# Kernel optimization log

Measured on AMD Instinct MI355X. Metric: run time of the kernel, lower is better.

The kernel has to match this reference:

```python
import jax, jax.numpy as jnp
import numpy as np

B, N, K = 4, 1024, 512
HEADS, DH = 8, 64
HID = 2048
KAPPA = 1.0      # kappa_beta
ALPHA = 1e-3     # ffn_alpha (prior weight)
LAM = 1.0        # ffn_lambda_belief
NITER = 2        # ffn_n_iterations
EPS = 1e-8


def _ln(x, g, b):
    m = jnp.mean(x, axis=-1, keepdims=True)
    v = jnp.var(x, axis=-1, keepdims=True)
    return (x - m) * jax.lax.rsqrt(v + 1e-5) * g + b


def _transport(x, phi, G):
    # truncated exp(phi . G) applied to x without materializing (B,N,K,K)
    def Ax(y):
        return jnp.einsum('bng,gkl,bnl->bnk', phi, G, y)
    a1 = Ax(x)
    return x + a1 + 0.5 * Ax(a1)


def setup_inputs() -> dict:
    key = jax.random.key(0)
    ks = jax.random.split(key, 16)
    mu_q = jax.random.normal(ks[0], (B, N, K), dtype=jnp.float32)
    sigma_q = jax.random.uniform(ks[1], (B, N, K), minval=0.5, maxval=1.5, dtype=jnp.float32)
    phi = 0.1 * jax.random.normal(ks[2], (B, N, 3), dtype=jnp.float32)
    A = jax.random.normal(ks[3], (3, K, K), dtype=jnp.float32)
    generators = 0.05 * (A - jnp.transpose(A, (0, 2, 1)))  # antisymmetric Lie generators
    mask = jnp.broadcast_to(jnp.tril(jnp.ones((N, N), dtype=bool)), (B, N, N))  # causal
    mu_prior = jax.random.normal(ks[4], (B, N, K), dtype=jnp.float32)
    s = 0.02
    Wq = s * jax.random.normal(ks[5], (K, K), dtype=jnp.float32)
    Wk = s * jax.random.normal(ks[6], (K, K), dtype=jnp.float32)
    Wv = s * jax.random.normal(ks[7], (K, K), dtype=jnp.float32)
    Wo = s * jax.random.normal(ks[8], (K, K), dtype=jnp.float32)
    g1 = jnp.ones((K,), jnp.float32); be1 = jnp.zeros((K,), jnp.float32)
    g2 = jnp.ones((K,), jnp.float32); be2 = jnp.zeros((K,), jnp.float32)
    W1 = s * jax.random.normal(ks[9], (K, HID), dtype=jnp.float32)
    bh1 = jnp.zeros((HID,), jnp.float32)
    W2 = s * jax.random.normal(ks[10], (HID, K), dtype=jnp.float32)
    bh2 = jnp.zeros((K,), jnp.float32)
    lr = jnp.array(0.1, jnp.float32)  # learnable VFE step size
    return {'mu_q': mu_q, 'sigma_q': sigma_q, 'phi': phi, 'generators': generators,
            'mask': mask, 'mu_prior': mu_prior, 'Wq': Wq, 'Wk': Wk, 'Wv': Wv, 'Wo': Wo,
            'g1': g1, 'be1': be1, 'g2': g2, 'be2': be2,
            'W1': W1, 'bh1': bh1, 'W2': W2, 'bh2': bh2, 'lr': lr}


def reference(mu_q, sigma_q, phi, generators, mask, mu_prior,
              Wq, Wk, Wv, Wo, g1, be1, g2, be2, W1, bh1, W2, bh2, lr):
    # ---- attention sublayer ----
    mu_n = _ln(mu_q, g1, be1)
    mu_g = _transport(mu_n, phi, generators)  # transport to common frame

    def heads(x):  # (B,N,K) -> (B,H,N,Dh)
        return x.reshape(B, N, HEADS, DH).transpose(0, 2, 1, 3)

    q = heads(mu_g @ Wq)
    k = heads(mu_g @ Wk)
    v = heads(mu_g @ Wv)
    # diagonal covariance propagated through linear maps: var_out = sigma @ W^2
    sq = heads(sigma_q @ (Wq * Wq)) + EPS
    sk = heads(sigma_q @ (Wk * Wk)) + EPS

    inv = 1.0 / sq
    # KL(N(k_j,sk_j) || N(q_i,sq_i)) for diagonal Gaussians, decomposed into matmuls
    tr = jnp.einsum('bhid,bhjd->bhij', inv, sk)
    quad = (jnp.sum(q * q * inv, axis=-1)[..., None]
            - 2.0 * jnp.einsum('bhid,bhjd->bhij', q * inv, k)
            + jnp.einsum('bhid,bhjd->bhij', inv, k * k))
    logdet = (jnp.sum(jnp.log(sq), axis=-1)[..., None]
              - jnp.sum(jnp.log(sk), axis=-1)[:, :, None, :])
    kl = 0.5 * (tr + quad - DH + logdet)  # (B,H,N,N)

    scores = jnp.where(mask[:, None, :, :], -kl / KAPPA, -1e9)
    beta = jax.nn.softmax(scores, axis=-1)

    out = jnp.einsum('bhij,bhjd->bhid', beta, v)
    out = out.transpose(0, 2, 1, 3).reshape(B, N, K)
    mu_attn = _transport(out @ Wo, -phi, generators)  # back-transport to local frames
    mu_res = mu_q + mu_attn  # residual (dropout is identity in eval)

    # ---- VFE_dynamic FFN sublayer ----
    mu_n2 = _ln(mu_res, g2, be2)
    beta_m = jnp.mean(beta, axis=1)  # (B,N,N) attention-belief coupling
    h = mu_n2
    for _ in range(NITER):
        drive = jax.nn.gelu(h @ W1 + bh1) @ W2 + bh2
        grad = ALPHA * (h - mu_prior) + LAM * (h - jnp.einsum('bij,bjk->bik', beta_m, h))
        h = h + lr * (drive - grad)
    mu_out = mu_res + (h - mu_n2)

    return (mu_out, sigma_q, phi)
```

## Files before the change

### kernel.cpp

```cpp
#include <hip/hip_runtime.h>
#include <math.h>

#define BB 4
#define NN 1024
#define KK 512
#define HH 8
#define DHh 64
#define HIDd 2048
#define BN (BB*NN)

typedef unsigned short u16;
typedef __attribute__((ext_vector_type(8))) short bf16x8;
typedef __attribute__((ext_vector_type(4))) float f32x4;

__device__ __forceinline__ float gelu_tanh(float x){
    float x3 = x*x*x;
    float t = tanhf(0.7978845608028654f*(x + 0.044715f*x3));
    return 0.5f*x*(1.0f+t);
}
__device__ __forceinline__ u16 f2bf(float x){
    unsigned int u = __float_as_uint(x);
    unsigned int r = (u + 0x7fffu + ((u>>16)&1u)) >> 16;
    return (u16)r;
}
__device__ __forceinline__ float bf2f(u16 b){
    return __uint_as_float(((unsigned int)b)<<16);
}
__device__ __forceinline__ void gload16(const void* g, void* l){
    __builtin_amdgcn_global_load_lds((__attribute__((address_space(1))) void*)g,
                                     (__attribute__((address_space(3))) void*)l, 16, 0, 0);
}
__device__ __forceinline__ void wsplit(u16* hi, u16* lo, size_t o, float v){
    u16 h = f2bf(v);
    hi[o] = h;
    if (lo) lo[o] = f2bf(v - bf2f(h));
}

__global__ __launch_bounds__(256) void split_t_k(
    const float* __restrict__ src, u16* __restrict__ hi, u16* __restrict__ lo,
    int Kc, int Nc, long sS, long sD, int square)
{
    __shared__ float t[32][33];
    const int n0 = blockIdx.x*32, k0 = blockIdx.y*32, bz = blockIdx.z;
    const float* S = src + (long)bz*sS;
    const int tx = threadIdx.x & 31, ty = threadIdx.x >> 5;
    for (int r = ty; r < 32; r += 8){
        float v = S[(long)(k0+r)*Nc + n0+tx];
        if (square) v *= v;
        t[r][tx] = v;
    }
    __syncthreads();
    for (int r = ty; r < 32; r += 8){
        float v = t[tx][r];
        long o = (long)bz*sD + (long)(n0+r)*Kc + k0 + tx;
        wsplit(hi, lo, o, v);
    }
}

__global__ __launch_bounds__(256) void wmega_k(
    const float* __restrict__ Wq, const float* __restrict__ Wk,
    const float* __restrict__ Wv, const float* __restrict__ Wo,
    const float* __restrict__ W1, const float* __restrict__ W2,
    const float* __restrict__ gen,
    u16* __restrict__ WQKVh, u16* __restrict__ WQKVl, u16* __restrict__ WoTh,
    u16* __restrict__ WSQKh, u16* __restrict__ WSQKl,
    u16* __restrict__ W1Th, u16* __restrict__ W2Th, u16* __restrict__ GFh)
{
    const int z = blockIdx.z;
    const int tid = threadIdx.x;
    if (z == 8){
        if (blockIdx.x >= 48) return;
        const int c0 = blockIdx.x*32, k0 = blockIdx.y*32;
        const int tx = tid&31, ty = tid>>5;
        const int g = c0/KK, l0 = c0%KK;
        for (int r=ty; r<32; r+=8)
            GFh[(size_t)(k0+r)*(3*KK) + c0+tx] =
                f2bf(gen[(size_t)g*KK*KK + (size_t)(k0+r)*KK + l0+tx]);
        return;
    }
    __shared__ float t[32][33];
    const float* src; u16* hi; u16* lo=0; int sq=0;
    int n0, k0, Kc, Nc;
    const size_t KK2 = (size_t)KK*KK;
    if (z < 6){
        if (blockIdx.x >= 16) return;
        n0 = blockIdx.x*32; k0 = blockIdx.y*32; Kc=KK; Nc=KK;
        if      (z==0){ src=Wq; hi=WQKVh;       lo=WQKVl; }
        else if (z==1){ src=Wk; hi=WQKVh+KK2;   lo=WQKVl+KK2; }
        else if (z==2){ src=Wv; hi=WQKVh+2*KK2; lo=WQKVl+2*KK2; }
        else if (z==3){ src=Wo; hi=WoTh; }
        else if (z==4){ src=Wq; hi=WSQKh;       lo=WSQKl; sq=1; }
        else          { src=Wk; hi=WSQKh+KK2;   lo=WSQKl+KK2; sq=1; }
    } else if (z == 6){
        src=W1; hi=W1Th; Kc=KK; Nc=HIDd;
        n0 = blockIdx.x*32; k0 = blockIdx.y*32;
    } else {
        src=W2; hi=W2Th; Kc=HIDd; Nc=KK;
        n0 = blockIdx.y*32; k0 = blockIdx.x*32;
    }
    const int tx=tid&31, ty=tid>>5;
    for (int r=ty;r<32;r+=8){
        float v = src[(long)(k0+r)*Nc + n0+tx];
        if (sq) v*=v;
        t[r][tx]=v;
    }
    __syncthreads();
    for (int r=ty;r<32;r+=8){
        float v = t[tx][r];
        long o = (long)(n0+r)*Kc + k0+tx;
        wsplit(hi, lo, o, v);
    }
}

template<int PRODS>
__global__ __launch_bounds__(256) void gemm_mfma_k(
    const u16* __restrict__ Ah, const u16* __restrict__ Al,
    const u16* __restrict__ Bh, const u16* __restrict__ Bl,
    float* __restrict__ C, u16* __restrict__ Chi, u16* __restrict__ Clo,
    int M, int Kc, int Nc, int lda,
    long sA, long sB, long sC, const float* __restrict__ bias, int act,
    int cskip)
{
    __shared__ u16 shAh[2][128*32], shBh[2][128*32];
    constexpr int SLO = (PRODS==3) ? 2*128*32 : 8;
    __shared__ u16 shAl[SLO], shBl[SLO];
    const int m0 = blockIdx.x*128, n0 = blockIdx.y*128;
    if (cskip == 1 && n0 > m0 + 127) return;
    const int bz = blockIdx.z;
    const u16* gAh = Ah + (long)bz*sA;
    const u16* gBh = Bh + (long)bz*sB;
    const u16* gAl = (PRODS==3) ? Al + (long)bz*sA : nullptr;
    const u16* gBl = (PRODS==3) ? Bl + (long)bz*sB : nullptr;
    const int tid = threadIdx.x;
    const int wave = tid >> 6, lane = tid & 63;
    const int quad = lane >> 4, r16 = lane & 15;
    const int wm = (wave>>1)*64, wn = (wave&1)*64;

    f32x4 acc[4][4];
    #pragma unroll
    for (int i=0;i<4;i++)
        #pragma unroll
        for (int j=0;j<4;j++) acc[i][j] = (f32x4){0.f,0.f,0.f,0.f};

    auto stage = [&](int sel, int k0){
        #pragma unroll
        for (int half=0; half<2; ++half){
            int c = half*256 + tid;
            int row = c >> 2;
            int kg = ((c & 3) ^ ((row >> 1) & 3))*8;
            long ga = (long)(m0+row)*lda + k0 + kg;
            long gb = (long)(n0+row)*Kc + k0 + kg;
            gload16(gAh+ga, &shAh[sel][c*8]);
            gload16(gBh+gb, &shBh[sel][c*8]);
            if constexpr (PRODS==3){
                gload16(gAl+ga, &shAl[sel*128*32 + c*8]);
                gload16(gBl+gb, &shBl[sel*128*32 + c*8]);
            }
        }
    };

    const int nsteps = Kc >> 5;
    stage(0, 0);
    __syncthreads();
    int cur = 0;
    const int swz = (quad ^ ((r16 >> 1) & 3))*8;
    for (int t = 0; t < nsteps; ++t){
        if (t+1 < nsteps) stage(cur^1, (t+1)<<5);
        bf16x8 afh[4], bfh[4];
        #pragma unroll
        for (int i=0;i<4;i++){
            afh[i] = *(const bf16x8*)&shAh[cur][(wm+i*16+r16)*32 + swz];
            bfh[i] = *(const bf16x8*)&shBh[cur][(wn+i*16+r16)*32 + swz];
        }
        if constexpr (PRODS==3){
            bf16x8 afl[4], bfl[4];
            #pragma unroll
            for (int i=0;i<4;i++){
                afl[i] = *(const bf16x8*)&shAl[cur*128*32 + (wm+i*16+r16)*32 + swz];
                bfl[i] = *(const bf16x8*)&shBl[cur*128*32 + (wn+i*16+r16)*32 + swz];
            }
            #pragma unroll
            for (int i=0;i<4;i++)
                #pragma unroll
                for (int j=0;j<4;j++){
                    acc[i][j] = __builtin_amdgcn_mfma_f32_16x16x32_bf16(afh[i], bfh[j], acc[i][j], 0,0,0);
                    acc[i][j] = __builtin_amdgcn_mfma_f32_16x16x32_bf16(afh[i], bfl[j], acc[i][j], 0,0,0);
                    acc[i][j] = __builtin_amdgcn_mfma_f32_16x16x32_bf16(afl[i], bfh[j], acc[i][j], 0,0,0);
                }
        } else {
            #pragma unroll
            for (int i=0;i<4;i++)
                #pragma unroll
                for (int j=0;j<4;j++)
                    acc[i][j] = __builtin_amdgcn_mfma_f32_16x16x32_bf16(afh[i], bfh[j], acc[i][j], 0,0,0);
        }
        __syncthreads();
        cur ^= 1;
    }
    #pragma unroll
    for (int i=0;i<4;i++){
        #pragma unroll
        for (int j=0;j<4;j++){
            int gc = n0 + wn + j*16 + r16;
            if (gc >= Nc) continue;
            float bv = bias ? bias[gc] : 0.f;
            #pragma unroll
            for (int r=0;r<4;r++){
                long gr = m0 + wm + i*16 + quad*4 + r;
                float v = acc[i][j][r] + bv;
                if (act) v = gelu_tanh(v);
                long o = (long)bz*sC + gr*Nc + gc;
                if (C) C[o] = v;
                if (Chi){ u16 t = f2bf(v); Chi[o] = t; if (Clo) Clo[o] = f2bf(v - bf2f(t)); }
            }
        }
    }
}

__global__ __launch_bounds__(256) void gemm64_k(
    const u16* __restrict__ Ah, const u16* __restrict__ Al,
    const u16* __restrict__ Bh, const u16* __restrict__ Bl,
    float* __restrict__ C, u16* __restrict__ Chi, u16* __restrict__ Clo,
    int M, int Kc, int Nc, int lda,
    long sA, long sB, long sC, const float* __restrict__ bias, int act,
    int ktrim, int prods,
    const float* __restrict__ phi, u16* __restrict__ X3e, float esign,
    const float* __restrict__ f_hin, const float* __restrict__ f_bmh,
    const float* __restrict__ f_mup, const float* __restrict__ f_lr,
    u16* __restrict__ f_hh, float* __restrict__ f_hout,
    const float* __restrict__ f_mrb, const float* __restrict__ f_mn2,
    float* __restrict__ f_out, int fmode)
{
    (void)Al; (void)Bl; (void)prods;
    __shared__ u16 shA[2][64*64], shB[2][64*64];
    const int m0 = blockIdx.x*64, n0 = blockIdx.y*64;
    const int bz = blockIdx.z;
    const u16* gA = Ah + (long)bz*sA;
    const u16* gB = Bh + (long)bz*sB;
    const int tid = threadIdx.x;
    const int wave = tid >> 6, lane = tid & 63;
    const int quad = lane >> 4, r16 = lane & 15;
    const int wr = wave*16;
    const int kend = ktrim ? min(Kc, m0 + 64) : Kc;
    const int nsteps = kend >> 6;

    f32x4 acc[4];
    #pragma unroll
    for (int j=0;j<4;j++) acc[j] = (f32x4){0.f,0.f,0.f,0.f};

    auto stage = [&](int sel, int k0){
        #pragma unroll
        for (int rep=0; rep<2; ++rep){
            int c = rep*256 + tid;
            int row = c >> 3;
            int kg = ((c & 7) ^ (row & 7))*8;
            gload16(gA + (long)(m0+row)*lda + k0 + kg, &shA[sel][c*8]);
            gload16(gB + (long)(n0+row)*Kc + k0 + kg, &shB[sel][c*8]);
        }
    };

    stage(0, 0);
    __syncthreads();
    int cur = 0;
    for (int t = 0; t < nsteps; ++t){
        if (t+1 < nsteps) stage(cur^1, (t+1)<<6);
        #pragma unroll
        for (int kk=0; kk<2; ++kk){
            const int s = (((kk<<2)+quad) ^ (r16 & 7))*8;
            bf16x8 af = *(const bf16x8*)&shA[cur][(wr+r16)*64 + s];
            #pragma unroll
            for (int j=0;j<4;j++){
                bf16x8 bh = *(const bf16x8*)&shB[cur][(j*16+r16)*64 + s];
                acc[j] = __builtin_amdgcn_mfma_f32_16x16x32_bf16(af, bh, acc[j], 0,0,0);
            }
        }
        __syncthreads();
        cur ^= 1;
    }
    float lrv = 0.f;
    if (fmode) lrv = *f_lr;
    #pragma unroll
    for (int j=0;j<4;j++){
        int gc = n0 + j*16 + r16;
        float bv = bias ? bias[gc] : 0.f;
        #pragma unroll
        for (int r=0;r<4;r++){
            long gr = m0 + wr + quad*4 + r;
            float v = acc[j][r] + bv;
            if (act) v = gelu_tanh(v);
            long o = (long)bz*sC + gr*Nc + gc;
            if (fmode){
                float hv = f_hin[o];
                float val = hv + lrv*(v - (1e-3f*(hv - f_mup[o]) + (hv - f_bmh[o])));
                if (fmode == 1){ f_hout[o] = val; f_hh[o] = f2bf(val); }
                else           { f_out[o] = f_mrb[o] + val - f_mn2[o]; }
            } else {
                if (C) C[o] = v;
                if (Chi){ u16 t = f2bf(v); Chi[o] = t; if (Clo) Clo[o] = f2bf(v - bf2f(t)); }
                if (X3e){
                    const float* ph = phi + gr*3;
                    size_t b = (size_t)gr*(3*KK) + gc;
                    X3e[b]      = f2bf(esign*ph[0]*v);
                    X3e[b+KK]   = f2bf(esign*ph[1]*v);
                    X3e[b+2*KK] = f2bf(esign*ph[2]*v);
                }
            }
        }
    }
}

__global__ __launch_bounds__(256) void ln_k(
    const float* __restrict__ x, const float* __restrict__ g,
    const float* __restrict__ be, float* __restrict__ y,
    const float* __restrict__ phi, u16* __restrict__ x3, float esign,
    const float* __restrict__ sg, u16* __restrict__ sgh, u16* __restrict__ sgl)
{
    __shared__ float sh[8];
    const int r = blockIdx.x, tid = threadIdx.x;
    const float* xr = x + (long)r*KK;
    float2 v = *(const float2*)(xr + tid*2);
    float s = v.x+v.y, s2 = v.x*v.x+v.y*v.y;
    #pragma unroll
    for (int o=32;o>0;o>>=1){ s += __shfl_down(s,o); s2 += __shfl_down(s2,o); }
    if ((tid&63)==0){ sh[tid>>6]=s; sh[4+(tid>>6)]=s2; }
    __syncthreads();
    s  = sh[0]+sh[1]+sh[2]+sh[3];
    s2 = sh[4]+sh[5]+sh[6]+sh[7];
    const float mean = s*(1.f/KK);
    const float var  = s2*(1.f/KK) - mean*mean;
    const float rs = rsqrtf(var + 1e-5f);
    float2 gg = *(const float2*)(g + tid*2);
    float2 bb = *(const float2*)(be + tid*2);
    float ox = (v.x-mean)*rs*gg.x + bb.x;
    float oy = (v.y-mean)*rs*gg.y + bb.y;
    long o = (long)r*KK + tid*2;
    *(float2*)(y + o) = make_float2(ox, oy);
    if (x3){
        const float* ph = phi + r*3;
        size_t b = (size_t)r*(3*KK) + tid*2;
        #pragma unroll
        for (int gg2=0; gg2<3; ++gg2){
            float p = esign*ph[gg2];
            x3[b + gg2*KK]     = f2bf(p*ox);
            x3[b + gg2*KK + 1] = f2bf(p*oy);
        }
    }
    if (sgh){
        float2 sv = *(const float2*)(sg + o);
        wsplit(sgh, sgl, o,   sv.x);
        wsplit(sgh, sgl, o+1, sv.y);
    }
}

__global__ __launch_bounds__(256) void resln_k(
    const float* __restrict__ wo, const float* __restrict__ a1,
    const float* __restrict__ a2, const float* __restrict__ res,
    const float* __restrict__ g, const float* __restrict__ be,
    float* __restrict__ mrb, float* __restrict__ mn2, u16* __restrict__ yh)
{
    __shared__ float sh[8];
    const int r = blockIdx.x, tid = threadIdx.x;
    long o = (long)r*KK + tid*2;
    float2 xv = *(const float2*)(wo + o);
    float2 v1 = *(const float2*)(a1 + o);
    float2 v2 = *(const float2*)(a2 + o);
    float2 rv = *(const float2*)(res + o);
    float mx = xv.x + v1.x + 0.5f*v2.x + rv.x;
    float my = xv.y + v1.y + 0.5f*v2.y + rv.y;
    *(float2*)(mrb + o) = make_float2(mx, my);
    float s = mx+my, s2 = mx*mx+my*my;
    #pragma unroll
    for (int of=32;of>0;of>>=1){ s += __shfl_down(s,of); s2 += __shfl_down(s2,of); }
    if ((tid&63)==0){ sh[tid>>6]=s; sh[4+(tid>>6)]=s2; }
    __syncthreads();
    s  = sh[0]+sh[1]+sh[2]+sh[3];
    s2 = sh[4]+sh[5]+sh[6]+sh[7];
    const float mean = s*(1.f/KK);
    const float var  = s2*(1.f/KK) - mean*mean;
    const float rs = rsqrtf(var + 1e-5f);
    float2 gg = *(const float2*)(g + tid*2);
    float2 bb = *(const float2*)(be + tid*2);
    float ox = (mx-mean)*rs*gg.x + bb.x;
    float oy = (my-mean)*rs*gg.y + bb.y;
    *(float2*)(mn2 + o) = make_float2(ox, oy);
    yh[o] = f2bf(ox); yh[o+1] = f2bf(oy);
}

__global__ void tfinal_k(const float* __restrict__ x, const float* __restrict__ a1,
                         const float* __restrict__ a2,
                         float* __restrict__ out, u16* __restrict__ oh, u16* __restrict__ ol){
    int i = blockIdx.x*256 + threadIdx.x;
    if (i >= BN*KK/4) return;
    float4 xv = ((const float4*)x)[i];
    float4 v1 = ((const float4*)a1)[i];
    float4 v2 = ((const float4*)a2)[i];
    float4 o;
    o.x = xv.x + v1.x + 0.5f*v2.x;
    o.y = xv.y + v1.y + 0.5f*v2.y;
    o.z = xv.z + v1.z + 0.5f*v2.z;
    o.w = xv.w + v1.w + 0.5f*v2.w;
    ((float4*)out)[i] = o;
    long ob = (long)i*4;
    wsplit(oh, ol, ob+0, o.x); wsplit(oh, ol, ob+1, o.y);
    wsplit(oh, ol, ob+2, o.z); wsplit(oh, ol, ob+3, o.w);
}
__global__ void outcopy_k(const float* __restrict__ sigma, const float* __restrict__ phi,
                          float* __restrict__ out){
    int i = blockIdx.x*256 + threadIdx.x;
    const int NS = BN*KK/4;
    if (i < NS){
        ((float4*)(out + (size_t)BN*KK))[i] = ((const float4*)sigma)[i];
    } else if (i < NS + BN*3/4){
        int j = i - NS;
        ((float4*)(out + 2*(size_t)BN*KK))[j] = ((const float4*)phi)[j];
    }
}

__global__ __launch_bounds__(512) void prepvt_k(
    const float* __restrict__ QKV, const float* __restrict__ SQSK,
    u16* __restrict__ CFh, u16* __restrict__ CFl,
    u16* __restrict__ KSh, u16* __restrict__ KSl, float* __restrict__ dvec,
    u16* __restrict__ VTh)
{
    __shared__ float t[64][65];
    const int bx = blockIdx.x;
    const int tid = threadIdx.x;
    if (bx < BN){
        const int bn = bx;
        const int b = bn / NN, n = bn % NN;
        const int h = tid >> 6, d = tid & 63;
        float q  = QKV[(size_t)bn*1536 + h*DHh + d];
        float k  = QKV[(size_t)bn*1536 + KK + h*DHh + d];
        float sq = SQSK[(size_t)bn*1024 + h*DHh + d] + 1e-8f;
        float sk = SQSK[(size_t)bn*1024 + KK + h*DHh + d] + 1e-8f;
        float inv = 1.f/sq;
        float nqi = -2.f*q*inv;
        float skk = sk + k*k;
        const size_t base = ((size_t)(h*BB + b)*NN + n)*128;
        wsplit(CFh, CFl, base+d,    inv);
        wsplit(CFh, CFl, base+64+d, nqi);
        wsplit(KSh, KSl, base+d,    skk);
        wsplit(KSh, KSl, base+64+d, k);
        float dv = __logf(sk);
        #pragma unroll
        for (int o=32;o>0;o>>=1) dv += __shfl_down(dv,o);
        if (d==0) dvec[((size_t)h*BB + b)*NN + n] = dv;
        return;
    }
    const int idx = bx - BN;
    const int n0 = (idx & 15)*64;
    const int h = (idx>>4)&7;
    const int b = idx>>7;
    const int c4 = (tid & 15) * 4;
    const int r0 = tid >> 4;
    for (int rr = r0; rr < 64; rr += 32){
        float4 v = *(const float4*)(QKV + (size_t)(b*NN + n0 + rr)*1536 + 1024 + h*DHh + c4);
        t[c4+0][rr] = v.x; t[c4+1][rr] = v.y; t[c4+2][rr] = v.z; t[c4+3][rr] = v.w;
    }
    __syncthreads();
    for (int dd = r0; dd < 64; dd += 32){
        size_t base = ((size_t)(h*BB + b)*64 + dd)*NN + n0 + c4;
        #pragma unroll
        for (int q=0;q<4;q++) VTh[base+q] = f2bf(t[dd][c4+q]);
    }
}

__global__ __launch_bounds__(256) void softmax2_k(
    float* __restrict__ S, const float* __restrict__ dvec,
    float* __restrict__ betam, u16* __restrict__ BMh, int g)
{
    __shared__ float s_sc[NN];
    __shared__ float s_bm[NN];
    __shared__ float s_red[4];
    const int tid = threadIdx.x;
    const int b = blockIdx.x / NN, i = blockIdx.x % NN;
    const int L = i + 1;
    const int JEND = ((i >> 6) + 1) << 6;
    for (int j=tid;j<JEND;j+=256) s_bm[j]=0.f;
    for (int hg=0; hg<4; ++hg){
        const int z = hg*BB + b;
        float* row = S + ((long)z*NN + i)*NN;
        const float* dp = dvec + ((size_t)(g*4+hg)*BB + b)*NN;
        float lm = -3.0e38f;
        for (int j=tid;j<L;j+=256){
            float sc = -0.5f*row[j] + 0.5f*dp[j];
            s_sc[j] = sc;
            lm = fmaxf(lm, sc);
        }
        #pragma unroll
        for (int o=32;o>0;o>>=1) lm = fmaxf(lm, __shfl_xor(lm, o));
        __syncthreads();
        if ((tid&63)==0) s_red[tid>>6] = lm;
        __syncthreads();
        const float mx = fmaxf(fmaxf(s_red[0],s_red[1]), fmaxf(s_red[2],s_red[3]));
        float ps = 0.f;
        for (int j=tid;j<L;j+=256){
            float e = __expf(s_sc[j]-mx);
            s_sc[j] = e;
            ps += e;
        }
        #pragma unroll
        for (int o=32;o>0;o>>=1) ps += __shfl_xor(ps, o);
        __syncthreads();
        if ((tid&63)==0) s_red[tid>>6] = ps;
        __syncthreads();
        const float isum = 1.f/(s_red[0]+s_red[1]+s_red[2]+s_red[3]);
        u16* brow = (u16*)row;
        for (int j=tid;j<JEND;j+=256){
            if (j < L){
                float w = s_sc[j]*isum;
                brow[j] = f2bf(w);
                s_bm[j] += 0.125f*w;
            } else {
                brow[j] = 0;
            }
        }
        __syncthreads();
    }
    const long bmrow = ((long)b*NN + i)*NN;
    if (g == 0){
        for (int j=tid;j<JEND;j+=256) betam[bmrow+j] = s_bm[j];
    } else {
        for (int j=tid;j<JEND;j+=256) BMh[bmrow+j] = f2bf(betam[bmrow+j] + s_bm[j]);
    }
}

__global__ __launch_bounds__(256) void pv_k(
    const u16* __restrict__ Sbeta,
    const u16* __restrict__ VTh,
    u16* __restrict__ xh, int g)
{
    __shared__ u16 shA[2][64*64], shB[2][64*64];
    const int m0 = blockIdx.x*64;
    const int z16 = blockIdx.y;
    const int b = z16 & 3, hg = z16 >> 2;
    const int head = g*4 + hg;
    const int vtz = head*BB + b;
    const int tid = threadIdx.x;
    const int wave = tid>>6, lane = tid&63;
    const int quad = lane>>4, r16 = lane&15;
    f32x4 acc[4];
    #pragma unroll
    for (int j=0;j<4;j++) acc[j]=(f32x4){0.f,0.f,0.f,0.f};
    const int nsteps = (m0 >> 6) + 1;

    auto stage = [&](int sel, int j0){
        #pragma unroll
        for (int rep=0; rep<2; ++rep){
            int c = rep*256 + tid;
            int row = c >> 3;
            int k8 = ((c & 7) ^ (row & 7))*8;
            gload16(Sbeta + ((size_t)(z16*NN + m0 + row))*(2*NN) + j0 + k8, &shA[sel][c*8]);
            gload16(VTh + ((size_t)(vtz*64 + row))*NN + j0 + k8, &shB[sel][c*8]);
        }
    };

    stage(0, 0);
    __syncthreads();
    int cur = 0;
    for (int t = 0; t < nsteps; ++t){
        if (t+1 < nsteps) stage(cur^1, (t+1)<<6);
        #pragma unroll
        for (int kk=0; kk<2; ++kk){
            const int s = (((kk<<2)+quad) ^ (r16 & 7))*8;
            bf16x8 af = *(const bf16x8*)&shA[cur][(wave*16 + r16)*64 + s];
            #pragma unroll
            for (int nj=0; nj<4; ++nj){
                bf16x8 bh = *(const bf16x8*)&shB[cur][(nj*16 + r16)*64 + s];
                acc[nj] = __builtin_amdgcn_mfma_f32_16x16x32_bf16(af, bh, acc[nj], 0,0,0);
            }
        }
        __syncthreads();
        cur ^= 1;
    }
    #pragma unroll
    for (int nj=0;nj<4;nj++){
        #pragma unroll
        for (int r=0;r<4;r++){
            int i = m0 + wave*16 + quad*4 + r;
            int d = nj*16 + r16;
            size_t o = ((size_t)(b*NN)+i)*KK + head*64 + d;
            xh[o] = f2bf(acc[nj][r]);
        }
    }
}

extern "C" void kernel_launch(void* const* d_in, const int* in_sizes, int n_in,
                              void* d_out, int out_size, void* d_ws, size_t ws_size,
                              hipStream_t stream) {
    const float* mu_q    = (const float*)d_in[0];
    const float* sigma_q = (const float*)d_in[1];
    const float* phi     = (const float*)d_in[2];
    const float* gen     = (const float*)d_in[3];
    const float* mu_prior= (const float*)d_in[5];
    const float* Wq = (const float*)d_in[6];
    const float* Wk = (const float*)d_in[7];
    const float* Wv = (const float*)d_in[8];
    const float* Wo = (const float*)d_in[9];
    const float* g1 = (const float*)d_in[10];
    const float* be1= (const float*)d_in[11];
    const float* g2 = (const float*)d_in[12];
    const float* be2= (const float*)d_in[13];
    const float* W1 = (const float*)d_in[14];
    const float* bh1= (const float*)d_in[15];
    const float* W2 = (const float*)d_in[16];
    const float* bh2= (const float*)d_in[17];
    const float* lr = (const float*)d_in[18];
    float* out = (float*)d_out;

    float* w = (float*)d_ws;
    size_t off = 0;
    auto alloc = [&](size_t n){ float* p = w + off; off += (n+3)&~(size_t)3; return p; };
    auto ualloc = [&](size_t n){ return (u16*)alloc((n+1)/2); };

    float* Xb   = alloc((size_t)BN*KK);
    float* A1b  = alloc((size_t)BN*KK);
    float* A2b  = alloc((size_t)BN*KK);
    float* QKVb = alloc((size_t)BN*3*KK);
    float* SQSKb= alloc((size_t)BN*2*KK);
    float* REG  = alloc((size_t)16*NN*NN);
    float* Sbuf = REG;
    u16*  X3a   = (u16*)REG;
    u16*  X3b   = X3a + (size_t)BN*3*KK;
    u16*  SGh   = X3b + (size_t)BN*3*KK;
    u16*  SGl   = SGh + (size_t)BN*KK;
    u16*  ZH    = (u16*)REG;
    float* Db_  = alloc((size_t)HH*BB*NN);
    float* BMb  = alloc((size_t)BB*NN*NN);
    u16* AH  = ualloc((size_t)BN*HIDd); u16* AL  = ualloc((size_t)BN*HIDd);
    u16* CFh = AH;
    u16* CFl = AH + (size_t)HH*BB*NN*128;
    u16* KSh = AL;
    u16* KSl = AL + (size_t)HH*BB*NN*128;
    u16* VTh = ualloc((size_t)HH*BB*64*NN);
    u16* GFh = ualloc((size_t)3*KK*KK);
    u16* WQKVh= ualloc((size_t)3*KK*KK); u16* WQKVl= ualloc((size_t)3*KK*KK);
    u16* WSQKh= ualloc((size_t)2*KK*KK); u16* WSQKl= ualloc((size_t)2*KK*KK);
    u16* WoTh= ualloc((size_t)KK*KK);
    u16* W1Th= ualloc((size_t)KK*HIDd);
    u16* W2Th= ualloc((size_t)KK*HIDd);
    u16* BMh = ualloc((size_t)BB*NN*NN);
    u16* HTh = ualloc((size_t)BB*KK*NN);
    float* WOb = QKVb;
    float* Hb  = QKVb + (size_t)BN*KK;
    float* MRb = QKVb + 2*(size_t)BN*KK;
    float* MN2b= Xb;

    auto gemm64 = [&](const u16* ah, const u16* al, const u16* bh, const u16* bl,
                      float* C, u16* chi, u16* clo, int M, int Kc, int Nc, int lda,
                      long sA, long sB, long sC, const float* bias, int act,
                      int ktrim, int prods, const float* xphi, u16* x3e, float esign,
                      int batch){
        dim3 g(M/64, Nc/64, batch);
        gemm64_k<<<g, 256, 0, stream>>>(ah, al, bh, bl, C, chi, clo,
                                        M, Kc, Nc, lda, sA, sB, sC, bias, act, ktrim, prods,
                                        xphi, x3e, esign,
                                        0,0,0,0,0,0,0,0,0,0);
    };
    const int EW = BN*KK/4/256;

    {
        dim3 gw(64, 16, 9);
        wmega_k<<<gw, 256, 0, stream>>>(Wq, Wk, Wv, Wo, W1, W2, gen,
                                        WQKVh, WQKVl, WoTh, WSQKh, WSQKl,
                                        W1Th, W2Th, GFh);
    }

    ln_k<<<BN, 256, 0, stream>>>(mu_q, g1, be1, Xb, phi, X3a, 1.f, sigma_q, SGh, SGl);
    gemm64(X3a, X3a, GFh, GFh, A1b, 0,0, BN, 3*KK, KK, 3*KK, 0,0,0, nullptr, 0, 0, 1,
           phi, X3b, 1.f, 1);
    gemm64(X3b, X3b, GFh, GFh, A2b, 0,0, BN, 3*KK, KK, 3*KK, 0,0,0, nullptr, 0, 0, 1,
           0, 0, 0.f, 1);
    tfinal_k<<<EW, 256, 0, stream>>>(Xb, A1b, A2b, Xb, AH, AL);

    {
        dim3 gq(BN/128, (3*KK)/128, 1);
        gemm_mfma_k<3><<<gq, 256, 0, stream>>>(AH, AL, WQKVh, WQKVl, QKVb, 0, 0,
            BN, KK, 3*KK, KK, 0, 0, 0, nullptr, 0, 0);
        dim3 gs(BN/128, (2*KK)/128, 1);
        gemm_mfma_k<3><<<gs, 256, 0, stream>>>(SGh, SGl, WSQKh, WSQKl, SQSKb, 0, 0,
            BN, KK, 2*KK, KK, 0, 0, 0, nullptr, 0, 0);
    }
    prepvt_k<<<BN + 512, 512, 0, stream>>>(QKVb, SQSKb, CFh, CFl, KSh, KSl, Db_, VTh);

    for (int g = 0; g < 2; ++g){
        size_t cfo = (size_t)g*4*BB*NN*128;
        dim3 sg(NN/128, NN/128, 16);
        gemm_mfma_k<3><<<sg, 256, 0, stream>>>(CFh+cfo, CFl+cfo, KSh+cfo, KSl+cfo,
            Sbuf, 0, 0, NN, 128, NN, 128,
            (long)NN*128, (long)NN*128, (long)NN*NN, nullptr, 0, 1);
        softmax2_k<<<BB*NN, 256, 0, stream>>>(Sbuf, Db_, BMb, BMh, g);
        dim3 pg(NN/64, 16, 1);
        pv_k<<<pg, 256, 0, stream>>>((const u16*)Sbuf, VTh, AH, g);
    }

    gemm64(AH, AH, WoTh, WoTh, WOb, 0,0, BN, KK, KK, KK, 0,0,0, nullptr, 0, 0, 1,
           phi, X3a, -1.f, 1);
    gemm64(X3a, X3a, GFh, GFh, A1b, 0,0, BN, 3*KK, KK, 3*KK, 0,0,0, nullptr, 0, 0, 1,
           phi, X3b, -1.f, 1);
    gemm64(X3b, X3b, GFh, GFh, A2b, 0,0, BN, 3*KK, KK, 3*KK, 0,0,0, nullptr, 0, 0, 1,
           0, 0, 0.f, 1);
    resln_k<<<BN, 256, 0, stream>>>(WOb, A1b, A2b, mu_q, g2, be2, MRb, MN2b, AH);

    for (int it=0; it<2; ++it){
        const float* hin = (it==0) ? MN2b : Hb;
        {
            dim3 tg(KK/32, NN/32, BB);
            split_t_k<<<tg, 256, 0, stream>>>(hin, HTh, 0, NN, KK,
                                              (long)NN*KK, (long)KK*NN, 0);
        }
        {
            dim3 bg(NN/64, KK/64, BB);
            gemm64_k<<<bg, 256, 0, stream>>>(BMh, BMh, HTh, HTh, A1b, 0,0,
                                             NN, NN, KK, NN,
                                             (long)NN*NN, (long)KK*NN, (long)NN*KK,
                                             nullptr, 0, 1, 1, 0, 0, 0.f,
                                             0,0,0,0,0,0,0,0,0,0);
        }
        {
            dim3 wg1(BN/128, HIDd/128, 1);
            gemm_mfma_k<1><<<wg1, 256, 0, stream>>>(AH, 0, W1Th, 0, 0, ZH, 0,
                BN, KK, HIDd, KK, 0, 0, 0, bh1, 1, 0);
        }
        {
            dim3 wg(BN/64, KK/64, 1);
            gemm64_k<<<wg, 256, 0, stream>>>(ZH, ZH, W2Th, W2Th, 0,0,0,
                                             BN, HIDd, KK, HIDd, 0,0,0, bh2, 0, 0, 1,
                                             0, 0, 0.f,
                                             hin, A1b, mu_prior, lr, AH, Hb, MRb, MN2b, out,
                                             (it==0) ? 1 : 2);
        }
    }

    outcopy_k<<<(BN*KK/4 + BN*3/4 + 255)/256, 256, 0, stream>>>(sigma_q, phi, out);

    (void)in_sizes; (void)n_in; (void)out_size; (void)ws_size;
}
```

Before: 650.2 us.

## Fuse transport epilogues into GEMMs and process all heads in one attention pass

Folds the transport-final combine (x + a1 + 0.5*a2, plus residual) into the second transport GEMM's epilogue, removing the tfinal and resln kernels. Reuses ln_k for the second layernorm, and has it also copy sigma and phi into the output, which drops outcopy_k. Merges the two 4-head attention groups into a single 32-batch score GEMM, softmax over all 8 heads, and PV launch, using a larger score buffer aliased onto Xb and removing the fp32 beta-mean staging buffer. In exchange, the score buffer is twice as large and now aliases other workspace, and there are more epilogue loads inside the GEMM.

```diff
diff --git a/kernel.cpp b/kernel.cpp
--- a/kernel.cpp
+++ b/kernel.cpp
@@ -218,20 +218,20 @@
 }
 
 __global__ __launch_bounds__(256) void gemm64_k(
-    const u16* __restrict__ Ah, const u16* __restrict__ Al,
-    const u16* __restrict__ Bh, const u16* __restrict__ Bl,
+    const u16* __restrict__ Ah, const u16* __restrict__ Bh,
     float* __restrict__ C, u16* __restrict__ Chi, u16* __restrict__ Clo,
     int M, int Kc, int Nc, int lda,
     long sA, long sB, long sC, const float* __restrict__ bias, int act,
-    int ktrim, int prods,
+    int ktrim,
     const float* __restrict__ phi, u16* __restrict__ X3e, float esign,
+    const float* __restrict__ t_x, const float* __restrict__ t_a1,
+    const float* __restrict__ t_res,
     const float* __restrict__ f_hin, const float* __restrict__ f_bmh,
     const float* __restrict__ f_mup, const float* __restrict__ f_lr,
     u16* __restrict__ f_hh, float* __restrict__ f_hout,
     const float* __restrict__ f_mrb, const float* __restrict__ f_mn2,
     float* __restrict__ f_out, int fmode)
 {
-    (void)Al; (void)Bl; (void)prods;
     __shared__ u16 shA[2][64*64], shB[2][64*64];
     const int m0 = blockIdx.x*64, n0 = blockIdx.y*64;
     const int bz = blockIdx.z;
@@ -289,6 +289,10 @@
             float v = acc[j][r] + bv;
             if (act) v = gelu_tanh(v);
             long o = (long)bz*sC + gr*Nc + gc;
+            if (t_x){
+                v = t_x[o] + t_a1[o] + 0.5f*v;
+                if (t_res) v += t_res[o];
+            }
             if (fmode){
                 float hv = f_hin[o];
                 float val = hv + lrv*(v - (1e-3f*(hv - f_mup[o]) + (hv - f_bmh[o])));
@@ -313,7 +317,8 @@
     const float* __restrict__ x, const float* __restrict__ g,
     const float* __restrict__ be, float* __restrict__ y,
     const float* __restrict__ phi, u16* __restrict__ x3, float esign,
-    const float* __restrict__ sg, u16* __restrict__ sgh, u16* __restrict__ sgl)
+    const float* __restrict__ sg, u16* __restrict__ sgh, u16* __restrict__ sgl,
+    u16* __restrict__ yh16, float* __restrict__ osig, float* __restrict__ ophi)
 {
     __shared__ float sh[8];
     const int r = blockIdx.x, tid = threadIdx.x;
@@ -335,6 +340,7 @@
     float oy = (v.y-mean)*rs*gg.y + bb.y;
     long o = (long)r*KK + tid*2;
     *(float2*)(y + o) = make_float2(ox, oy);
+    if (yh16){ yh16[o] = f2bf(ox); yh16[o+1] = f2bf(oy); }
     if (x3){
         const float* ph = phi + r*3;
         size_t b = (size_t)r*(3*KK) + tid*2;
@@ -344,75 +350,13 @@
             x3[b + gg2*KK]     = f2bf(p*ox);
             x3[b + gg2*KK + 1] = f2bf(p*oy);
         }
+        if (ophi && tid < 3) ophi[(size_t)r*3 + tid] = phi[(size_t)r*3 + tid];
     }
     if (sgh){
         float2 sv = *(const float2*)(sg + o);
         wsplit(sgh, sgl, o,   sv.x);
         wsplit(sgh, sgl, o+1, sv.y);
-    }
-}
-
-__global__ __launch_bounds__(256) void resln_k(
-    const float* __restrict__ wo, const float* __restrict__ a1,
-    const float* __restrict__ a2, const float* __restrict__ res,
-    const float* __restrict__ g, const float* __restrict__ be,
-    float* __restrict__ mrb, float* __restrict__ mn2, u16* __restrict__ yh)
-{
-    __shared__ float sh[8];
-    const int r = blockIdx.x, tid = threadIdx.x;
-    long o = (long)r*KK + tid*2;
-    float2 xv = *(const float2*)(wo + o);
-    float2 v1 = *(const float2*)(a1 + o);
-    float2 v2 = *(const float2*)(a2 + o);
-    float2 rv = *(const float2*)(res + o);
-    float mx = xv.x + v1.x + 0.5f*v2.x + rv.x;
-    float my = xv.y + v1.y + 0.5f*v2.y + rv.y;
-    *(float2*)(mrb + o) = make_float2(mx, my);
-    float s = mx+my, s2 = mx*mx+my*my;
-    #pragma unroll
-    for (int of=32;of>0;of>>=1){ s += __shfl_down(s,of); s2 += __shfl_down(s2,of); }
-    if ((tid&63)==0){ sh[tid>>6]=s; sh[4+(tid>>6)]=s2; }
-    __syncthreads();
-    s  = sh[0]+sh[1]+sh[2]+sh[3];
-    s2 = sh[4]+sh[5]+sh[6]+sh[7];
-    const float mean = s*(1.f/KK);
-    const float var  = s2*(1.f/KK) - mean*mean;
-    const float rs = rsqrtf(var + 1e-5f);
-    float2 gg = *(const float2*)(g + tid*2);
-    float2 bb = *(const float2*)(be + tid*2);
-    float ox = (mx-mean)*rs*gg.x + bb.x;
-    float oy = (my-mean)*rs*gg.y + bb.y;
-    *(float2*)(mn2 + o) = make_float2(ox, oy);
-    yh[o] = f2bf(ox); yh[o+1] = f2bf(oy);
-}
-
-__global__ void tfinal_k(const float* __restrict__ x, const float* __restrict__ a1,
-                         const float* __restrict__ a2,
-                         float* __restrict__ out, u16* __restrict__ oh, u16* __restrict__ ol){
-    int i = blockIdx.x*256 + threadIdx.x;
-    if (i >= BN*KK/4) return;
-    float4 xv = ((const float4*)x)[i];
-    float4 v1 = ((const float4*)a1)[i];
-    float4 v2 = ((const float4*)a2)[i];
-    float4 o;
-    o.x = xv.x + v1.x + 0.5f*v2.x;
-    o.y = xv.y + v1.y + 0.5f*v2.y;
-    o.z = xv.z + v1.z + 0.5f*v2.z;
-    o.w = xv.w + v1.w + 0.5f*v2.w;
-    ((float4*)out)[i] = o;
-    long ob = (long)i*4;
-    wsplit(oh, ol, ob+0, o.x); wsplit(oh, ol, ob+1, o.y);
-    wsplit(oh, ol, ob+2, o.z); wsplit(oh, ol, ob+3, o.w);
-}
-__global__ void outcopy_k(const float* __restrict__ sigma, const float* __restrict__ phi,
-                          float* __restrict__ out){
-    int i = blockIdx.x*256 + threadIdx.x;
-    const int NS = BN*KK/4;
-    if (i < NS){
-        ((float4*)(out + (size_t)BN*KK))[i] = ((const float4*)sigma)[i];
-    } else if (i < NS + BN*3/4){
-        int j = i - NS;
-        ((float4*)(out + 2*(size_t)BN*KK))[j] = ((const float4*)phi)[j];
+        if (osig) *(float2*)(osig + o) = sv;
     }
 }
 
@@ -465,9 +409,8 @@
     }
 }
 
-__global__ __launch_bounds__(256) void softmax2_k(
-    float* __restrict__ S, const float* __restrict__ dvec,
-    float* __restrict__ betam, u16* __restrict__ BMh, int g)
+__global__ __launch_bounds__(256) void softmax_all_k(
+    float* __restrict__ S, const float* __restrict__ dvec, u16* __restrict__ BMh)
 {
     __shared__ float s_sc[NN];
     __shared__ float s_bm[NN];
@@ -477,10 +420,10 @@
     const int L = i + 1;
     const int JEND = ((i >> 6) + 1) << 6;
     for (int j=tid;j<JEND;j+=256) s_bm[j]=0.f;
-    for (int hg=0; hg<4; ++hg){
-        const int z = hg*BB + b;
+    for (int h=0; h<8; ++h){
+        const int z = h*BB + b;
         float* row = S + ((long)z*NN + i)*NN;
-        const float* dp = dvec + ((size_t)(g*4+hg)*BB + b)*NN;
+        const float* dp = dvec + (size_t)z*NN;
         float lm = -3.0e38f;
         for (int j=tid;j<L;j+=256){
             float sc = -0.5f*row[j] + 0.5f*dp[j];
@@ -518,24 +461,18 @@
         __syncthreads();
     }
     const long bmrow = ((long)b*NN + i)*NN;
-    if (g == 0){
-        for (int j=tid;j<JEND;j+=256) betam[bmrow+j] = s_bm[j];
-    } else {
-        for (int j=tid;j<JEND;j+=256) BMh[bmrow+j] = f2bf(betam[bmrow+j] + s_bm[j]);
-    }
+    for (int j=tid;j<JEND;j+=256) BMh[bmrow+j] = f2bf(s_bm[j]);
 }
 
 __global__ __launch_bounds__(256) void pv_k(
     const u16* __restrict__ Sbeta,
     const u16* __restrict__ VTh,
-    u16* __restrict__ xh, int g)
+    u16* __restrict__ xh)
 {
     __shared__ u16 shA[2][64*64], shB[2][64*64];
     const int m0 = blockIdx.x*64;
-    const int z16 = blockIdx.y;
-    const int b = z16 & 3, hg = z16 >> 2;
-    const int head = g*4 + hg;
-    const int vtz = head*BB + b;
+    const int z = blockIdx.y;
+    const int b = z & 3, head = z >> 2;
     const int tid = threadIdx.x;
     const int wave = tid>>6, lane = tid&63;
     const int quad = lane>>4, r16 = lane&15;
@@ -550,8 +487,8 @@
             int c = rep*256 + tid;
             int row = c >> 3;
             int k8 = ((c & 7) ^ (row & 7))*8;
-            gload16(Sbeta + ((size_t)(z16*NN + m0 + row))*(2*NN) + j0 + k8, &shA[sel][c*8]);
-            gload16(VTh + ((size_t)(vtz*64 + row))*NN + j0 + k8, &shB[sel][c*8]);
+            gload16(Sbeta + ((size_t)(z*NN + m0 + row))*(2*NN) + j0 + k8, &shA[sel][c*8]);
+            gload16(VTh + ((size_t)(z*64 + row))*NN + j0 + k8, &shB[sel][c*8]);
         }
     };
 
@@ -619,14 +556,13 @@
     float* QKVb = alloc((size_t)BN*3*KK);
     float* SQSKb= alloc((size_t)BN*2*KK);
     float* REG  = alloc((size_t)16*NN*NN);
-    float* Sbuf = REG;
+    float* Sbig = Xb;
     u16*  X3a   = (u16*)REG;
     u16*  X3b   = X3a + (size_t)BN*3*KK;
     u16*  SGh   = X3b + (size_t)BN*3*KK;
     u16*  SGl   = SGh + (size_t)BN*KK;
     u16*  ZH    = (u16*)REG;
     float* Db_  = alloc((size_t)HH*BB*NN);
-    float* BMb  = alloc((size_t)BB*NN*NN);
     u16* AH  = ualloc((size_t)BN*HIDd); u16* AL  = ualloc((size_t)BN*HIDd);
     u16* CFh = AH;
     u16* CFl = AH + (size_t)HH*BB*NN*128;
@@ -645,19 +581,19 @@
     float* Hb  = QKVb + (size_t)BN*KK;
     float* MRb = QKVb + 2*(size_t)BN*KK;
     float* MN2b= Xb;
-
-    auto gemm64 = [&](const u16* ah, const u16* al, const u16* bh, const u16* bl,
+    (void)A2b; (void)SQSKb;
+
+    auto gemm64 = [&](const u16* ah, const u16* bh,
                       float* C, u16* chi, u16* clo, int M, int Kc, int Nc, int lda,
                       long sA, long sB, long sC, const float* bias, int act,
-                      int ktrim, int prods, const float* xphi, u16* x3e, float esign,
-                      int batch){
+                      int ktrim, const float* xphi, u16* x3e, float esign,
+                      const float* tx, const float* ta1, const float* tres, int batch){
         dim3 g(M/64, Nc/64, batch);
-        gemm64_k<<<g, 256, 0, stream>>>(ah, al, bh, bl, C, chi, clo,
-                                        M, Kc, Nc, lda, sA, sB, sC, bias, act, ktrim, prods,
-                                        xphi, x3e, esign,
+        gemm64_k<<<g, 256, 0, stream>>>(ah, bh, C, chi, clo,
+                                        M, Kc, Nc, lda, sA, sB, sC, bias, act, ktrim,
+                                        xphi, x3e, esign, tx, ta1, tres,
                                         0,0,0,0,0,0,0,0,0,0);
     };
-    const int EW = BN*KK/4/256;
 
     {
         dim3 gw(64, 16, 9);
@@ -666,12 +602,12 @@
                                         W1Th, W2Th, GFh);
     }
 
-    ln_k<<<BN, 256, 0, stream>>>(mu_q, g1, be1, Xb, phi, X3a, 1.f, sigma_q, SGh, SGl);
-    gemm64(X3a, X3a, GFh, GFh, A1b, 0,0, BN, 3*KK, KK, 3*KK, 0,0,0, nullptr, 0, 0, 1,
-           phi, X3b, 1.f, 1);
-    gemm64(X3b, X3b, GFh, GFh, A2b, 0,0, BN, 3*KK, KK, 3*KK, 0,0,0, nullptr, 0, 0, 1,
-           0, 0, 0.f, 1);
-    tfinal_k<<<EW, 256, 0, stream>>>(Xb, A1b, A2b, Xb, AH, AL);
+    ln_k<<<BN, 256, 0, stream>>>(mu_q, g1, be1, Xb, phi, X3a, 1.f, sigma_q, SGh, SGl,
+                                 0, out + (size_t)BN*KK, out + 2*(size_t)BN*KK);
+    gemm64(X3a, GFh, A1b, 0,0, BN, 3*KK, KK, 3*KK, 0,0,0, nullptr, 0, 0,
+           phi, X3b, 1.f, 0,0,0, 1);
+    gemm64(X3b, GFh, 0, AH, AL, BN, 3*KK, KK, 3*KK, 0,0,0, nullptr, 0, 0,
+           0, 0, 0.f, Xb, A1b, 0, 1);
 
     {
         dim3 gq(BN/128, (3*KK)/128, 1);
@@ -683,24 +619,24 @@
     }
     prepvt_k<<<BN + 512, 512, 0, stream>>>(QKVb, SQSKb, CFh, CFl, KSh, KSl, Db_, VTh);
 
-    for (int g = 0; g < 2; ++g){
-        size_t cfo = (size_t)g*4*BB*NN*128;
-        dim3 sg(NN/128, NN/128, 16);
-        gemm_mfma_k<3><<<sg, 256, 0, stream>>>(CFh+cfo, CFl+cfo, KSh+cfo, KSl+cfo,
-            Sbuf, 0, 0, NN, 128, NN, 128,
+    {
+        dim3 sg(NN/128, NN/128, 32);
+        gemm_mfma_k<3><<<sg, 256, 0, stream>>>(CFh, CFl, KSh, KSl,
+            Sbig, 0, 0, NN, 128, NN, 128,
             (long)NN*128, (long)NN*128, (long)NN*NN, nullptr, 0, 1);
-        softmax2_k<<<BB*NN, 256, 0, stream>>>(Sbuf, Db_, BMb, BMh, g);
-        dim3 pg(NN/64, 16, 1);
-        pv_k<<<pg, 256, 0, stream>>>((const u16*)Sbuf, VTh, AH, g);
-    }
-
-    gemm64(AH, AH, WoTh, WoTh, WOb, 0,0, BN, KK, KK, KK, 0,0,0, nullptr, 0, 0, 1,
-           phi, X3a, -1.f, 1);
-    gemm64(X3a, X3a, GFh, GFh, A1b, 0,0, BN, 3*KK, KK, 3*KK, 0,0,0, nullptr, 0, 0, 1,
-           phi, X3b, -1.f, 1);
-    gemm64(X3b, X3b, GFh, GFh, A2b, 0,0, BN, 3*KK, KK, 3*KK, 0,0,0, nullptr, 0, 0, 1,
-           0, 0, 0.f, 1);
-    resln_k<<<BN, 256, 0, stream>>>(WOb, A1b, A2b, mu_q, g2, be2, MRb, MN2b, AH);
+        softmax_all_k<<<BB*NN, 256, 0, stream>>>(Sbig, Db_, BMh);
+        dim3 pg(NN/64, 32, 1);
+        pv_k<<<pg, 256, 0, stream>>>((const u16*)Sbig, VTh, AH);
+    }
+
+    gemm64(AH, WoTh, WOb, 0,0, BN, KK, KK, KK, 0,0,0, nullptr, 0, 0,
+           phi, X3a, -1.f, 0,0,0, 1);
+    gemm64(X3a, GFh, A1b, 0,0, BN, 3*KK, KK, 3*KK, 0,0,0, nullptr, 0, 0,
+           phi, X3b, -1.f, 0,0,0, 1);
+    gemm64(X3b, GFh, MRb, 0,0, BN, 3*KK, KK, 3*KK, 0,0,0, nullptr, 0, 0,
+           0, 0, 0.f, WOb, A1b, mu_q, 1);
+    ln_k<<<BN, 256, 0, stream>>>(MRb, g2, be2, MN2b, 0, 0, 0.f, 0, 0, 0,
+                                 AH, 0, 0);
 
     for (int it=0; it<2; ++it){
         const float* hin = (it==0) ? MN2b : Hb;
@@ -711,10 +647,10 @@
         }
         {
             dim3 bg(NN/64, KK/64, BB);
-            gemm64_k<<<bg, 256, 0, stream>>>(BMh, BMh, HTh, HTh, A1b, 0,0,
+            gemm64_k<<<bg, 256, 0, stream>>>(BMh, HTh, A1b, 0,0,
                                              NN, NN, KK, NN,
                                              (long)NN*NN, (long)KK*NN, (long)NN*KK,
-                                             nullptr, 0, 1, 1, 0, 0, 0.f,
+                                             nullptr, 0, 1, 0, 0, 0.f, 0,0,0,
                                              0,0,0,0,0,0,0,0,0,0);
         }
         {
@@ -724,15 +660,13 @@
         }
         {
             dim3 wg(BN/64, KK/64, 1);
-            gemm64_k<<<wg, 256, 0, stream>>>(ZH, ZH, W2Th, W2Th, 0,0,0,
-                                             BN, HIDd, KK, HIDd, 0,0,0, bh2, 0, 0, 1,
-                                             0, 0, 0.f,
+            gemm64_k<<<wg, 256, 0, stream>>>(ZH, W2Th, 0,0,0,
+                                             BN, HIDd, KK, HIDd, 0,0,0, bh2, 0, 0,
+                                             0, 0, 0.f, 0,0,0,
                                              hin, A1b, mu_prior, lr, AH, Hb, MRb, MN2b, out,
                                              (it==0) ? 1 : 2);
         }
     }
 
-    outcopy_k<<<(BN*KK/4 + BN*3/4 + 255)/256, 256, 0, stream>>>(sigma_q, phi, out);
-
     (void)in_sizes; (void)n_in; (void)out_size; (void)ws_size;
 }
```

Measured after the change: 624.8 us. 3.9% less time.
